# Performance work log

Measured on AMD Instinct MI355X. Metric: run time of the kernel, lower is better.

Reference implementation:

```python
import jax, jax.numpy as jnp
import numpy as np

B, C, O, H, W = 4, 256, 256, 64, 64
KH = KW = 3
KK = KH * KW
PAD = 1  # stride=1, padding=1 -> output spatial == input spatial


def setup_inputs() -> dict:
    key = jax.random.key(0)
    k0, k1, k2, k3 = jax.random.split(key, 4)
    x = jax.random.normal(k0, (B, C, H, W), jnp.float32)
    # offset-predicting conv: small weights -> realistic sub-pixel offsets
    w_off = jax.random.normal(k1, (3 * KK, C, KH, KW), jnp.float32) * 0.01
    b_off = jnp.zeros((3 * KK,), jnp.float32)
    w_def = jax.random.normal(k2, (O, C, KH, KW), jnp.float32) * (1.0 / np.sqrt(C * KK))
    b_def = jax.random.normal(k3, (O,), jnp.float32) * 0.01
    return {"x": x, "w_off": w_off, "b_off": b_off, "w_def": w_def, "b_def": b_def}


def _conv2d(x, w, b):
    y = jax.lax.conv_general_dilated(
        x, w, window_strides=(1, 1), padding=((PAD, PAD), (PAD, PAD)),
        dimension_numbers=("NCHW", "OIHW", "NCHW"))
    return y + b[None, :, None, None]


def _deform_conv2d(x, offsets, mask, w, b):
    # torchvision modulated DeformConv2d, stride=1, pad=1, dilation=1.
    Bx, Cx, Hx, Wx = x.shape
    Ox = w.shape[0]
    # offsets: [B, 2*KK, H, W] with channel 2k = dy, 2k+1 = dx for tap k
    off = offsets.reshape(Bx, KK, 2, Hx, Wx)
    ky, kx = jnp.meshgrid(jnp.arange(KH), jnp.arange(KW), indexing="ij")
    ky = ky.reshape(KK)
    kx = kx.reshape(KK)
    base_y = (ky[:, None, None] - PAD + jnp.arange(Hx)[None, :, None]).astype(x.dtype)  # [KK,H,1]
    base_x = (kx[:, None, None] - PAD + jnp.arange(Wx)[None, None, :]).astype(x.dtype)  # [KK,1,W]
    sy = off[:, :, 0] + base_y  # [B,KK,H,W] sample rows
    sx = off[:, :, 1] + base_x  # [B,KK,H,W] sample cols

    y0 = jnp.floor(sy)
    x0 = jnp.floor(sx)
    ty = sy - y0  # fractional weights (grad flows to offsets through these)
    tx = sx - x0

    x_flat = x.reshape(Bx, Cx, Hx * Wx)
    val = jnp.zeros((Bx, Cx, KK, Hx, Wx), x.dtype)
    for dy in (0, 1):  # 4 bilinear corners (fixed small loop)
        for dx in (0, 1):
            yi = y0.astype(jnp.int32) + dy
            xi = x0.astype(jnp.int32) + dx
            wgt = (ty if dy else 1.0 - ty) * (tx if dx else 1.0 - tx)
            valid = (yi >= 0) & (yi < Hx) & (xi >= 0) & (xi < Wx)  # zero outside
            idx = (jnp.clip(yi, 0, Hx - 1) * Wx + jnp.clip(xi, 0, Wx - 1)).reshape(Bx, 1, -1)
            g = jnp.take_along_axis(x_flat, idx, axis=2).reshape(Bx, Cx, KK, Hx, Wx)
            val = val + g * jnp.where(valid, wgt, 0.0)[:, None]

    val = val * mask.reshape(Bx, 1, KK, Hx, Wx)  # modulation
    out = jnp.einsum("bckhw,ock->bohw", val, w.reshape(Ox, Cx, KK))
    return out + b[None, :, None, None]


def reference(x, w_off, b_off, w_def, b_def):
    pred = _conv2d(x, w_off, b_off)            # [B, 3*KK, H, W]
    offsets = pred[:, : 2 * KK]                # [B, 2*KK, H, W]
    mask = jax.nn.sigmoid(pred[:, 2 * KK:])    # [B, KK, H, W]
    return _deform_conv2d(x, offsets, mask, w_def, b_def)
```

## Files before the change

kernel.cpp:

```cpp
#include <hip/hip_runtime.h>

#define BB 4
#define CCH 256
#define OCH 256
#define HH 64
#define WW 64
#define HWSZ 4096

typedef __bf16 bf16_t;
typedef bf16_t bf16x8 __attribute__((ext_vector_type(8)));
typedef bf16_t bf16x2_t __attribute__((ext_vector_type(2)));
typedef float f32x4 __attribute__((ext_vector_type(4)));

__device__ __forceinline__ unsigned int packbf(float a, float b) {
    bf16x2_t p;
    p.x = (__bf16)a;
    p.y = (__bf16)b;
    return __builtin_bit_cast(unsigned int, p);
}
__device__ __forceinline__ float blo(unsigned int u) { return __uint_as_float(u << 16); }
__device__ __forceinline__ float bhi(unsigned int u) { return __uint_as_float(u & 0xFFFF0000u); }

__global__ __launch_bounds__(256) void k_prep(const float* __restrict__ x,
                                              const float* __restrict__ w_off,
                                              const float* __restrict__ w_def,
                                              const float* __restrict__ b_def,
                                              ushort* __restrict__ xT,
                                              ushort* __restrict__ w1F,
                                              ushort* __restrict__ w2F,
                                              float* __restrict__ P,
                                              float* __restrict__ out) {
    int bid = blockIdx.x;
    if (bid < 256) {
        int b = bid >> 6;
        int h = bid & 63;
        int tid = threadIdx.x;
        int wv = tid >> 6;
        int lane = tid & 63;

        __shared__ unsigned int buf[64][130];

        const float* xp = x + ((size_t)b * CCH + wv * 64) * HWSZ + h * WW + lane;
#pragma unroll 8
        for (int i = 0; i < 32; ++i) {
            float a = xp[(size_t)(2 * i) * HWSZ];
            float c = xp[(size_t)(2 * i + 1) * HWSZ];
            buf[lane][wv * 32 + i] = packbf(a, c);
        }
        __syncthreads();

        ushort* dst = xT + ((size_t)(b * 64 + h) * 64) * 256;
#pragma unroll
        for (int r = 0; r < 16; ++r) {
            int idx = tid + r * 256;
            int w = idx >> 6;
            int q = idx & 63;
            uint2 v = *(const uint2*)&buf[w][2 * q];
            *(uint2*)(dst + (size_t)w * 256 + q * 4) = v;
        }
        return;
    }

    int i = (bid - 256) * 256 + threadIdx.x;
    if (i < 73728) {
        int j = i & 7;
        int o = (i >> 3) & 31;
        int cSub = (i >> 8) & 31;
        int k = i >> 13;
        float v = 0.0f;
        if (o < 27) v = w_off[((size_t)o * CCH + cSub * 8 + j) * 9 + k];
        w1F[i] = (ushort)(packbf(v, 0.f) & 0xFFFFu);
        return;
    }
    i -= 73728;
    if (i < 589824) {
        int j = i & 7;
        int o = (i >> 3) & 255;
        int cg = (i >> 11) & 31;
        int k = i >> 16;
        float v = w_def[(size_t)o * 2304 + (cg * 8 + j) * 9 + k];
        w2F[i] = (ushort)(packbf(v, 0.f) & 0xFFFFu);
        return;
    }
    i -= 589824;
    if (i < 110592) {
        ((float4*)P)[i] = make_float4(0.f, 0.f, 0.f, 0.f);
        return;
    }
    i -= 110592;
    if (i < 1048576) {
        float v = b_def[(i >> 10) & 255];
        ((float4*)out)[i] = make_float4(v, v, v, v);
    }
}

__global__ __launch_bounds__(512) void k_pred4(const ushort* __restrict__ xT,
                                               const ushort* __restrict__ w1F,
                                               float* __restrict__ P) {
    int bid = blockIdx.x;
    int L = (bid & 7) * 64 + (bid >> 3);
    int cs = L & 3;
    int hg = (L >> 2) & 31;
    int b  = L >> 7;
    int tid = threadIdx.x;
    int lane = tid & 63;
    int wv   = tid >> 6;
    int l16  = lane & 15;
    int lq   = lane >> 4;
    int spx  = tid >> 3;
    int cl   = tid & 7;

    __shared__ ushort b_lds[2][8][8][16][8];

    const ushort* xTb = xT + (size_t)b * HWSZ * 256 + cs * 64 + cl * 8;
    const bf16x8* w1v = (const bf16x8*)w1F;

    f32x4 acc[2];
    acc[0] = (f32x4){0.f, 0.f, 0.f, 0.f};
    acc[1] = (f32x4){0.f, 0.f, 0.f, 0.f};

    auto stageLoad = [&](int k, int tpx) -> uint4 {
        int row = hg * 2 + (tpx >> 6);
        int col = tpx & 63;
        int ys = row + k / 3 - 1;
        int xs = col + k % 3 - 1;
        bool ok = (ys >= 0 && ys < HH && xs >= 0 && xs < WW);
        uint4 v = make_uint4(0u, 0u, 0u, 0u);
        if (ok) v = *(const uint4*)(xTb + (size_t)(ys * WW + xs) * 256);
        return v;
    };
    auto stageWrite = [&](uint4 v, int buf, int tpx) {
        *(uint4*)&b_lds[buf][cl][tpx >> 4][(tpx & 15) ^ cl][0] = v;
    };

    {
        uint4 v0 = stageLoad(0, spx);
        uint4 v1 = stageLoad(0, spx + 64);
        stageWrite(v0, 0, spx);
        stageWrite(v1, 0, spx + 64);
    }
    __syncthreads();

    for (int t = 0; t < 9; ++t) {
        int cur = t & 1;
        uint4 n0, n1;
        if (t < 8) {
            n0 = stageLoad(t + 1, spx);
            n1 = stageLoad(t + 1, spx + 64);
        }
        bf16x8 a00 = w1v[(size_t)(t * 32 + cs * 8 + 0 * 4 + lq) * 32 + 0 * 16 + l16];
        bf16x8 a01 = w1v[(size_t)(t * 32 + cs * 8 + 0 * 4 + lq) * 32 + 1 * 16 + l16];
        bf16x8 a10 = w1v[(size_t)(t * 32 + cs * 8 + 1 * 4 + lq) * 32 + 0 * 16 + l16];
        bf16x8 a11 = w1v[(size_t)(t * 32 + cs * 8 + 1 * 4 + lq) * 32 + 1 * 16 + l16];
        bf16x8 b0 = *(const bf16x8*)&b_lds[cur][0 * 4 + lq][wv][l16 ^ (0 * 4 + lq)][0];
        bf16x8 b1 = *(const bf16x8*)&b_lds[cur][1 * 4 + lq][wv][l16 ^ (1 * 4 + lq)][0];
        acc[0] = __builtin_amdgcn_mfma_f32_16x16x32_bf16(a00, b0, acc[0], 0, 0, 0);
        acc[1] = __builtin_amdgcn_mfma_f32_16x16x32_bf16(a01, b0, acc[1], 0, 0, 0);
        acc[0] = __builtin_amdgcn_mfma_f32_16x16x32_bf16(a10, b1, acc[0], 0, 0, 0);
        acc[1] = __builtin_amdgcn_mfma_f32_16x16x32_bf16(a11, b1, acc[1], 0, 0, 0);
        if (t < 8) {
            stageWrite(n0, cur ^ 1, spx);
            stageWrite(n1, cur ^ 1, spx + 64);
        }
        __syncthreads();
    }

    int prow = hg * 2 + (wv >> 2);
    int pcol = (wv & 3) * 16 + l16;
#pragma unroll
    for (int mf = 0; mf < 2; ++mf) {
#pragma unroll
        for (int r = 0; r < 4; ++r) {
            int o = mf * 16 + lq * 4 + r;
            if (o < 27) {
                atomicAdd(&P[((size_t)b * 27 + o) * HWSZ + prow * WW + pcol],
                          acc[mf][r]);
            }
        }
    }
}

__global__ __launch_bounds__(512, 4) void k_deform8(const ushort* __restrict__ xT,
                                                    const float* __restrict__ P,
                                                    const float* __restrict__ b_off,
                                                    const ushort* __restrict__ w2F,
                                                    float* __restrict__ out) {
    int bid = blockIdx.x;
    int L = (bid & 7) * 64 + (bid >> 3);
    int cs = L & 1;
    int h  = (L >> 1) & 63;
    int b  = L >> 7;
    int tid = threadIdx.x;
    int lane = tid & 63;
    int wv   = tid >> 6;
    int l16  = lane & 15;
    int lq   = lane >> 4;
    int px   = tid >> 3;
    int cl   = tid & 7;

    __shared__ ushort b_lds[2][8][4][16][8];

    const char* xTc = (const char*)xT + (size_t)b * HWSZ * 512 + cs * 256 + cl * 16;
    const bf16x8* w2b = (const bf16x8*)w2F + (size_t)(cs * 16) * 256 + wv * 32 + l16;

    uint4* wdst0 = (uint4*)&b_lds[0][cl][px >> 4][(px & 15) ^ cl][0];
    uint4* wdst1 = (uint4*)&b_lds[1][cl][px >> 4][(px & 15) ^ cl][0];

    f32x4 acc[2][4];
#pragma unroll
    for (int mf = 0; mf < 2; ++mf)
#pragma unroll
        for (int nt = 0; nt < 4; ++nt) acc[mf][nt] = (f32x4){0.f, 0.f, 0.f, 0.f};

    const float* Pb = P + (size_t)b * 27 * HWSZ + h * WW + px;

    float pOy, pOx, pMr, bOy, bOx, bMr;
    float wgt[4];
    const char* aptr[4];

    auto loadP = [&](int k) {
        pOy = Pb[(size_t)(2 * k) * HWSZ];
        pOx = Pb[(size_t)(2 * k + 1) * HWSZ];
        pMr = Pb[(size_t)(18 + k) * HWSZ];
        bOy = b_off[2 * k];
        bOx = b_off[2 * k + 1];
        bMr = b_off[18 + k];
    };
    auto calcDesc = [&](int k) {
        float offy = pOy + bOy;
        float offx = pOx + bOx;
        float m = 1.0f / (1.0f + expf(-(pMr + bMr)));
        float sy = offy + (float)(h + k / 3 - 1);
        float sx = offx + (float)(px + k % 3 - 1);
        float y0f = floorf(sy), x0f = floorf(sx);
        float ty = sy - y0f, tx = sx - x0f;
        int y0 = (int)y0f, x0 = (int)x0f;
#pragma unroll
        for (int dy = 0; dy < 2; ++dy) {
#pragma unroll
            for (int dx = 0; dx < 2; ++dx) {
                int yi = y0 + dy, xi = x0 + dx;
                bool ok = (yi >= 0 && yi < HH && xi >= 0 && xi < WW);
                float wg = (dy ? ty : 1.0f - ty) * (dx ? tx : 1.0f - tx) * m;
                wgt[dy * 2 + dx]  = ok ? wg : 0.0f;
                aptr[dy * 2 + dx] = xTc + (size_t)(ok ? (yi * WW + xi) : 0) * 512;
            }
        }
    };

    uint4 gbA[4], gbB[4];
    float wgtA[4], wgtB[4];
    bf16x8 aA[2][2], aB[2][2];

    auto issueGatherTo = [&](uint4 (&gb)[4], float (&wg)[4], int off) {
#pragma unroll
        for (int c = 0; c < 4; ++c) gb[c] = *(const uint4*)(aptr[c] + off);
#pragma unroll
        for (int c = 0; c < 4; ++c) wg[c] = wgt[c];
    };
    auto combineFrom = [&](const uint4 (&g)[4], const float (&w)[4]) -> uint4 {
        uint4 r;
        {
            float lo = w[0]*blo(g[0].x) + w[1]*blo(g[1].x) + w[2]*blo(g[2].x) + w[3]*blo(g[3].x);
            float hi = w[0]*bhi(g[0].x) + w[1]*bhi(g[1].x) + w[2]*bhi(g[2].x) + w[3]*bhi(g[3].x);
            r.x = packbf(lo, hi);
        }
        {
            float lo = w[0]*blo(g[0].y) + w[1]*blo(g[1].y) + w[2]*blo(g[2].y) + w[3]*blo(g[3].y);
            float hi = w[0]*bhi(g[0].y) + w[1]*bhi(g[1].y) + w[2]*bhi(g[2].y) + w[3]*bhi(g[3].y);
            r.y = packbf(lo, hi);
        }
        {
            float lo = w[0]*blo(g[0].z) + w[1]*blo(g[1].z) + w[2]*blo(g[2].z) + w[3]*blo(g[3].z);
            float hi = w[0]*bhi(g[0].z) + w[1]*bhi(g[1].z) + w[2]*bhi(g[2].z) + w[3]*bhi(g[3].z);
            r.z = packbf(lo, hi);
        }
        {
            float lo = w[0]*blo(g[0].w) + w[1]*blo(g[1].w) + w[2]*blo(g[2].w) + w[3]*blo(g[3].w);
            float hi = w[0]*bhi(g[0].w) + w[1]*bhi(g[1].w) + w[2]*bhi(g[2].w) + w[3]*bhi(g[3].w);
            r.w = packbf(lo, hi);
        }
        return r;
    };
    auto loadATo = [&](bf16x8 (&a)[2][2], int t) {
        size_t base = ((size_t)((t >> 1) * 32 + (t & 1) * 8) + lq) * 256;
#pragma unroll
        for (int g = 0; g < 2; ++g)
#pragma unroll
            for (int mf = 0; mf < 2; ++mf)
                a[mf][g] = w2b[base + (size_t)g * 1024 + mf * 16];
    };

#define MFMA_BODY(BUF, AREG)                                                        \
    do {                                                                            \
        bf16x8 bfr[2][4];                                                           \
        _Pragma("unroll")                                                           \
        for (int g = 0; g < 2; ++g) {                                               \
            int kg = g * 4 + lq;                                                    \
            _Pragma("unroll")                                                       \
            for (int nt = 0; nt < 4; ++nt)                                          \
                bfr[g][nt] = *(const bf16x8*)&b_lds[BUF][kg][nt][l16 ^ kg][0];      \
        }                                                                           \
        _Pragma("unroll")                                                           \
        for (int g = 0; g < 2; ++g)                                                 \
            _Pragma("unroll")                                                       \
            for (int mf = 0; mf < 2; ++mf)                                          \
                _Pragma("unroll")                                                   \
                for (int nt = 0; nt < 4; ++nt)                                      \
                    acc[mf][nt] = __builtin_amdgcn_mfma_f32_16x16x32_bf16(          \
                        AREG[mf][g], bfr[g][nt], acc[mf][nt], 0, 0, 0);             \
    } while (0)

    loadP(0);
    calcDesc(0);
    issueGatherTo(gbA, wgtA, 0);
    issueGatherTo(gbB, wgtB, 128);
    loadP(1);
    loadATo(aA, 0);
    *wdst0 = combineFrom(gbA, wgtA);
    __syncthreads();

    for (int tp = 0; tp < 9; ++tp) {
        if (tp < 8) {
            calcDesc(tp + 1);
            issueGatherTo(gbA, wgtA, 0);
        }
        loadATo(aB, 2 * tp + 1);
        MFMA_BODY(0, aA);
        *wdst1 = combineFrom(gbB, wgtB);
        __syncthreads();

        if (tp < 8) {
            issueGatherTo(gbB, wgtB, 128);
            if (tp < 7) loadP(tp + 2);
            loadATo(aA, 2 * tp + 2);
        }
        MFMA_BODY(1, aB);
        if (tp < 8) {
            *wdst0 = combineFrom(gbA, wgtA);
        }
        __syncthreads();
    }
#undef MFMA_BODY

#pragma unroll
    for (int mf = 0; mf < 2; ++mf) {
#pragma unroll
        for (int nt = 0; nt < 4; ++nt) {
#pragma unroll
            for (int r = 0; r < 4; ++r) {
                int o = wv * 32 + mf * 16 + lq * 4 + r;
                atomicAdd(&out[((size_t)b * OCH + o) * HWSZ + h * WW + nt * 16 + l16],
                          acc[mf][nt][r]);
            }
        }
    }
}

extern "C" void kernel_launch(void* const* d_in, const int* in_sizes, int n_in,
                              void* d_out, int out_size, void* d_ws, size_t ws_size,
                              hipStream_t stream) {
    const float* x     = (const float*)d_in[0];
    const float* w_off = (const float*)d_in[1];
    const float* b_off = (const float*)d_in[2];
    const float* w_def = (const float*)d_in[3];
    const float* b_def = (const float*)d_in[4];
    float* out = (float*)d_out;

    float*  P   = (float*)d_ws;
    ushort* w1F = (ushort*)(P + (size_t)BB * 27 * HWSZ);
    ushort* w2F = w1F + 73728;
    ushort* xT  = w2F + 589824;

    hipLaunchKernelGGL(k_prep, dim3(7376), dim3(256), 0, stream,
                       x, w_off, w_def, b_def, xT, w1F, w2F, P, out);
    hipLaunchKernelGGL(k_pred4, dim3(512), dim3(512), 0, stream, xT, w1F, P);
    hipLaunchKernelGGL(k_deform8, dim3(512), dim3(512), 0, stream, xT, P, b_off, w2F, out);
}
```

Before: 82.57 us.

## Split deform kernel channel dimension four ways and double grid size

The deform conv kernel now splits the 256 input channels into four slices of 64 instead of two slices of 128, launching 1024 blocks instead of 512. Each block now iterates over the 9 taps with one 64-channel chunk per tap, so the pipeline is restructured to alternate taps between the two LDS buffers instead of alternating channel halves. This aims to raise parallelism and occupancy across CUs. The cost is recomputing the bilinear descriptors and offset loads in twice as many blocks, and twice as many atomic adds to the output.

```diff
diff --git a/kernel.cpp b/kernel.cpp
--- a/kernel.cpp
+++ b/kernel.cpp
@@ -180,16 +180,16 @@
     }
 }
 
-__global__ __launch_bounds__(512, 4) void k_deform8(const ushort* __restrict__ xT,
-                                                    const float* __restrict__ P,
-                                                    const float* __restrict__ b_off,
-                                                    const ushort* __restrict__ w2F,
-                                                    float* __restrict__ out) {
+__global__ __launch_bounds__(512, 4) void k_deform12(const ushort* __restrict__ xT,
+                                                     const float* __restrict__ P,
+                                                     const float* __restrict__ b_off,
+                                                     const ushort* __restrict__ w2F,
+                                                     float* __restrict__ out) {
     int bid = blockIdx.x;
-    int L = (bid & 7) * 64 + (bid >> 3);
-    int cs = L & 1;
-    int h  = (L >> 1) & 63;
-    int b  = L >> 7;
+    int L = (bid & 7) * 128 + (bid >> 3);
+    int cs = L & 3;
+    int h  = (L >> 2) & 63;
+    int b  = L >> 8;
     int tid = threadIdx.x;
     int lane = tid & 63;
     int wv   = tid >> 6;
@@ -200,8 +200,8 @@
 
     __shared__ ushort b_lds[2][8][4][16][8];
 
-    const char* xTc = (const char*)xT + (size_t)b * HWSZ * 512 + cs * 256 + cl * 16;
-    const bf16x8* w2b = (const bf16x8*)w2F + (size_t)(cs * 16) * 256 + wv * 32 + l16;
+    const char* xTc = (const char*)xT + (size_t)b * HWSZ * 512 + cs * 128 + cl * 16;
+    const bf16x8* w2b = (const bf16x8*)w2F + wv * 32 + l16;
 
     uint4* wdst0 = (uint4*)&b_lds[0][cl][px >> 4][(px & 15) ^ cl][0];
     uint4* wdst1 = (uint4*)&b_lds[1][cl][px >> 4][(px & 15) ^ cl][0];
@@ -252,9 +252,9 @@
     float wgtA[4], wgtB[4];
     bf16x8 aA[2][2], aB[2][2];
 
-    auto issueGatherTo = [&](uint4 (&gb)[4], float (&wg)[4], int off) {
-#pragma unroll
-        for (int c = 0; c < 4; ++c) gb[c] = *(const uint4*)(aptr[c] + off);
+    auto issueGatherTo = [&](uint4 (&gb)[4], float (&wg)[4]) {
+#pragma unroll
+        for (int c = 0; c < 4; ++c) gb[c] = *(const uint4*)(aptr[c]);
 #pragma unroll
         for (int c = 0; c < 4; ++c) wg[c] = wgt[c];
     };
@@ -283,7 +283,7 @@
         return r;
     };
     auto loadATo = [&](bf16x8 (&a)[2][2], int t) {
-        size_t base = ((size_t)((t >> 1) * 32 + (t & 1) * 8) + lq) * 256;
+        size_t base = ((size_t)(t * 32 + cs * 8) + lq) * 256;
 #pragma unroll
         for (int g = 0; g < 2; ++g)
 #pragma unroll
@@ -313,34 +313,35 @@
 
     loadP(0);
     calcDesc(0);
-    issueGatherTo(gbA, wgtA, 0);
-    issueGatherTo(gbB, wgtB, 128);
+    issueGatherTo(gbA, wgtA);
     loadP(1);
+    calcDesc(1);
+    issueGatherTo(gbB, wgtB);
+    loadP(2);
     loadATo(aA, 0);
     *wdst0 = combineFrom(gbA, wgtA);
     __syncthreads();
 
-    for (int tp = 0; tp < 9; ++tp) {
-        if (tp < 8) {
-            calcDesc(tp + 1);
-            issueGatherTo(gbA, wgtA, 0);
-        }
+    for (int tp = 0; tp < 4; ++tp) {
+        calcDesc(2 * tp + 2);
+        issueGatherTo(gbA, wgtA);
+        if (tp < 3) loadP(2 * tp + 3);
         loadATo(aB, 2 * tp + 1);
         MFMA_BODY(0, aA);
         *wdst1 = combineFrom(gbB, wgtB);
         __syncthreads();
 
-        if (tp < 8) {
-            issueGatherTo(gbB, wgtB, 128);
-            if (tp < 7) loadP(tp + 2);
-            loadATo(aA, 2 * tp + 2);
-        }
+        if (tp < 3) {
+            calcDesc(2 * tp + 3);
+            issueGatherTo(gbB, wgtB);
+            loadP(2 * tp + 4);
+        }
+        loadATo(aA, 2 * tp + 2);
         MFMA_BODY(1, aB);
-        if (tp < 8) {
-            *wdst0 = combineFrom(gbA, wgtA);
-        }
+        *wdst0 = combineFrom(gbA, wgtA);
         __syncthreads();
     }
+    MFMA_BODY(0, aA);
 #undef MFMA_BODY
 
 #pragma unroll
@@ -375,5 +376,5 @@
     hipLaunchKernelGGL(k_prep, dim3(7376), dim3(256), 0, stream,
                        x, w_off, w_def, b_def, xT, w1F, w2F, P, out);
     hipLaunchKernelGGL(k_pred4, dim3(512), dim3(512), 0, stream, xT, w1F, P);
-    hipLaunchKernelGGL(k_deform8, dim3(512), dim3(512), 0, stream, xT, P, b_off, w2F, out);
-}
+    hipLaunchKernelGGL(k_deform12, dim3(1024), dim3(512), 0, stream, xT, P, b_off, w2F, out);
+}
```

Measured after the change: 94.32 us. 14.2% more time.

## Split deform blocks by pixel half instead of channel half, drop output atomics

Applied to the files above, without the earlier changes.

The deformable-conv kernel now assigns each block half a row of pixels across all 256 input channels, rather than all 64 pixels across half the channels. Each block then owns its output tile completely and can write results plus bias directly instead of using atomicAdd. This removes the bias-initialisation pass over the output in the prep kernel, so the prep grid is smaller. Each block now gathers more channels per pixel and holds larger A-fragment register arrays, which may raise register pressure. An unused block_sync helper is also added.

```diff
diff --git a/kernel.cpp b/kernel.cpp
--- a/kernel.cpp
+++ b/kernel.cpp
@@ -21,15 +21,19 @@
 __device__ __forceinline__ float blo(unsigned int u) { return __uint_as_float(u << 16); }
 __device__ __forceinline__ float bhi(unsigned int u) { return __uint_as_float(u & 0xFFFF0000u); }
 
+__device__ __forceinline__ void block_sync() {
+    asm volatile("s_waitcnt lgkmcnt(0)" ::: "memory");
+    __builtin_amdgcn_s_barrier();
+    __builtin_amdgcn_sched_barrier(0);
+}
+
 __global__ __launch_bounds__(256) void k_prep(const float* __restrict__ x,
                                               const float* __restrict__ w_off,
                                               const float* __restrict__ w_def,
-                                              const float* __restrict__ b_def,
                                               ushort* __restrict__ xT,
                                               ushort* __restrict__ w1F,
                                               ushort* __restrict__ w2F,
-                                              float* __restrict__ P,
-                                              float* __restrict__ out) {
+                                              float* __restrict__ P) {
     int bid = blockIdx.x;
     if (bid < 256) {
         int b = bid >> 6;
@@ -85,12 +89,6 @@
     i -= 589824;
     if (i < 110592) {
         ((float4*)P)[i] = make_float4(0.f, 0.f, 0.f, 0.f);
-        return;
-    }
-    i -= 110592;
-    if (i < 1048576) {
-        float v = b_def[(i >> 10) & 255];
-        ((float4*)out)[i] = make_float4(v, v, v, v);
     }
 }
 
@@ -180,39 +178,41 @@
     }
 }
 
-__global__ __launch_bounds__(512, 4) void k_deform8(const ushort* __restrict__ xT,
-                                                    const float* __restrict__ P,
-                                                    const float* __restrict__ b_off,
-                                                    const ushort* __restrict__ w2F,
-                                                    float* __restrict__ out) {
+__global__ __launch_bounds__(512, 4) void k_deform15(const ushort* __restrict__ xT,
+                                                     const float* __restrict__ P,
+                                                     const float* __restrict__ b_off,
+                                                     const ushort* __restrict__ w2F,
+                                                     const float* __restrict__ b_def,
+                                                     float* __restrict__ out) {
     int bid = blockIdx.x;
     int L = (bid & 7) * 64 + (bid >> 3);
-    int cs = L & 1;
+    int ph = L & 1;
     int h  = (L >> 1) & 63;
     int b  = L >> 7;
+    int px0 = ph * 32;
     int tid = threadIdx.x;
     int lane = tid & 63;
     int wv   = tid >> 6;
     int l16  = lane & 15;
     int lq   = lane >> 4;
-    int px   = tid >> 3;
-    int cl   = tid & 7;
-
-    __shared__ ushort b_lds[2][8][4][16][8];
-
-    const char* xTc = (const char*)xT + (size_t)b * HWSZ * 512 + cs * 256 + cl * 16;
-    const bf16x8* w2b = (const bf16x8*)w2F + (size_t)(cs * 16) * 256 + wv * 32 + l16;
-
-    uint4* wdst0 = (uint4*)&b_lds[0][cl][px >> 4][(px & 15) ^ cl][0];
-    uint4* wdst1 = (uint4*)&b_lds[1][cl][px >> 4][(px & 15) ^ cl][0];
-
-    f32x4 acc[2][4];
+    int pxs  = tid >> 4;
+    int cl   = tid & 15;
+
+    __shared__ ushort b_lds[2][16][2][16][8];
+
+    const char* xTc = (const char*)xT + (size_t)b * HWSZ * 512 + cl * 16;
+    const bf16x8* w2b = (const bf16x8*)w2F + wv * 32 + l16;
+
+    uint4* wdst0 = (uint4*)&b_lds[0][cl][pxs >> 4][(pxs & 15) ^ cl][0];
+    uint4* wdst1 = (uint4*)&b_lds[1][cl][pxs >> 4][(pxs & 15) ^ cl][0];
+
+    f32x4 acc[2][2];
 #pragma unroll
     for (int mf = 0; mf < 2; ++mf)
 #pragma unroll
-        for (int nt = 0; nt < 4; ++nt) acc[mf][nt] = (f32x4){0.f, 0.f, 0.f, 0.f};
-
-    const float* Pb = P + (size_t)b * 27 * HWSZ + h * WW + px;
+        for (int nt = 0; nt < 2; ++nt) acc[mf][nt] = (f32x4){0.f, 0.f, 0.f, 0.f};
+
+    const float* Pb = P + (size_t)b * 27 * HWSZ + h * WW + px0 + pxs;
 
     float pOy, pOx, pMr, bOy, bOx, bMr;
     float wgt[4];
@@ -231,7 +231,7 @@
         float offx = pOx + bOx;
         float m = 1.0f / (1.0f + expf(-(pMr + bMr)));
         float sy = offy + (float)(h + k / 3 - 1);
-        float sx = offx + (float)(px + k % 3 - 1);
+        float sx = offx + (float)(px0 + pxs + k % 3 - 1);
         float y0f = floorf(sy), x0f = floorf(sx);
         float ty = sy - y0f, tx = sx - x0f;
         int y0 = (int)y0f, x0 = (int)x0f;
@@ -250,7 +250,7 @@
 
     uint4 gbA[4], gbB[4];
     float wgtA[4], wgtB[4];
-    bf16x8 aA[2][2], aB[2][2];
+    bf16x8 aA[2][4], aB[2][4];
 
     auto issueGatherTo = [&](uint4 (&gb)[4], float (&wg)[4], int off) {
 #pragma unroll
@@ -282,10 +282,10 @@
         }
         return r;
     };
-    auto loadATo = [&](bf16x8 (&a)[2][2], int t) {
-        size_t base = ((size_t)((t >> 1) * 32 + (t & 1) * 8) + lq) * 256;
-#pragma unroll
-        for (int g = 0; g < 2; ++g)
+    auto loadATo = [&](bf16x8 (&a)[2][4], int t) {
+        size_t base = ((size_t)((t >> 1) * 32 + (t & 1) * 16) + lq) * 256;
+#pragma unroll
+        for (int g = 0; g < 4; ++g)
 #pragma unroll
             for (int mf = 0; mf < 2; ++mf)
                 a[mf][g] = w2b[base + (size_t)g * 1024 + mf * 16];
@@ -293,20 +293,20 @@
 
 #define MFMA_BODY(BUF, AREG)                                                        \
     do {                                                                            \
-        bf16x8 bfr[2][4];                                                           \
+        bf16x8 bfr[4][2];                                                           \
         _Pragma("unroll")                                                           \
-        for (int g = 0; g < 2; ++g) {                                               \
+        for (int g = 0; g < 4; ++g) {                                               \
             int kg = g * 4 + lq;                                                    \
             _Pragma("unroll")                                                       \
-            for (int nt = 0; nt < 4; ++nt)                                          \
+            for (int nt = 0; nt < 2; ++nt)                                          \
                 bfr[g][nt] = *(const bf16x8*)&b_lds[BUF][kg][nt][l16 ^ kg][0];      \
         }                                                                           \
         _Pragma("unroll")                                                           \
-        for (int g = 0; g < 2; ++g)                                                 \
+        for (int g = 0; g < 4; ++g)                                                 \
             _Pragma("unroll")                                                       \
             for (int mf = 0; mf < 2; ++mf)                                          \
                 _Pragma("unroll")                                                   \
-                for (int nt = 0; nt < 4; ++nt)                                      \
+                for (int nt = 0; nt < 2; ++nt)                                      \
                     acc[mf][nt] = __builtin_amdgcn_mfma_f32_16x16x32_bf16(          \
                         AREG[mf][g], bfr[g][nt], acc[mf][nt], 0, 0, 0);             \
     } while (0)
@@ -314,7 +314,7 @@
     loadP(0);
     calcDesc(0);
     issueGatherTo(gbA, wgtA, 0);
-    issueGatherTo(gbB, wgtB, 128);
+    issueGatherTo(gbB, wgtB, 256);
     loadP(1);
     loadATo(aA, 0);
     *wdst0 = combineFrom(gbA, wgtA);
@@ -331,7 +331,7 @@
         __syncthreads();
 
         if (tp < 8) {
-            issueGatherTo(gbB, wgtB, 128);
+            issueGatherTo(gbB, wgtB, 256);
             if (tp < 7) loadP(tp + 2);
             loadATo(aA, 2 * tp + 2);
         }
@@ -346,12 +346,12 @@
 #pragma unroll
     for (int mf = 0; mf < 2; ++mf) {
 #pragma unroll
-        for (int nt = 0; nt < 4; ++nt) {
+        for (int nt = 0; nt < 2; ++nt) {
 #pragma unroll
             for (int r = 0; r < 4; ++r) {
                 int o = wv * 32 + mf * 16 + lq * 4 + r;
-                atomicAdd(&out[((size_t)b * OCH + o) * HWSZ + h * WW + nt * 16 + l16],
-                          acc[mf][nt][r]);
+                out[((size_t)b * OCH + o) * HWSZ + h * WW + px0 + nt * 16 + l16] =
+                    acc[mf][nt][r] + b_def[o];
             }
         }
     }
@@ -372,8 +372,9 @@
     ushort* w2F = w1F + 73728;
     ushort* xT  = w2F + 589824;
 
-    hipLaunchKernelGGL(k_prep, dim3(7376), dim3(256), 0, stream,
-                       x, w_off, w_def, b_def, xT, w1F, w2F, P, out);
+    hipLaunchKernelGGL(k_prep, dim3(3280), dim3(256), 0, stream,
+                       x, w_off, w_def, xT, w1F, w2F, P);
     hipLaunchKernelGGL(k_pred4, dim3(512), dim3(512), 0, stream, xT, w1F, P);
-    hipLaunchKernelGGL(k_deform8, dim3(512), dim3(512), 0, stream, xT, P, b_off, w2F, out);
-}
+    hipLaunchKernelGGL(k_deform15, dim3(512), dim3(512), 0, stream,
+                       xT, P, b_off, w2F, b_def, out);
+}
```

After: 76.58 us. -7.3%, faster.
